# Kernel optimization log

Measured on AMD Instinct MI355X. Metric: run time of the kernel, lower is better.

Reference implementation:

```python
import jax, jax.numpy as jnp
import numpy as np

N_NODES = 100000
N_REL = 5
IN_F = 128
HID = 128

def _glorot(key, shape):
    fan_in, fan_out = shape[-2], shape[-1]
    s = jnp.sqrt(6.0 / (fan_in + fan_out))
    return jax.random.uniform(key, shape, jnp.float32, -s, s)

def setup_inputs() -> dict:
    key = jax.random.key(0)
    ks = jax.random.split(key, 16)
    x = jax.random.normal(ks[0], (N_NODES, IN_F), jnp.float32)
    edge_index = jax.random.randint(ks[1], (2, 1600000), 0, N_NODES, jnp.int32)
    edge_type = jax.random.randint(ks[2], (1600000,), 0, N_REL, jnp.int32)
    d = {"x": x, "edge_index": edge_index, "edge_type": edge_type}
    dims = [(IN_F, HID), (HID, HID), (HID, HID)]
    for li, (fi, fo) in enumerate(dims, start=1):
        d[f"W{li}"] = _glorot(ks[3 * li], (N_REL, fi, fo))        # per-relation weights
        d[f"root{li}"] = _glorot(ks[3 * li + 1], (fi, fo))        # root/self weight
        d[f"b{li}"] = jnp.zeros((fo,), jnp.float32)               # bias
    return d

def _rgcn_conv(x, src, dst, edge_type, W, root, b):
    # out = x @ root + b + sum_r segment_mean_r(x[src] @ W_r -> dst)
    out = x @ root + b
    for r in range(N_REL):  # small fixed relation count
        m = (edge_type == r).astype(x.dtype)                      # [E]
        h = (x @ W[r])[src] * m[:, None]                          # [E, out]
        s = jax.ops.segment_sum(h, dst, num_segments=N_NODES)     # [N, out]
        c = jax.ops.segment_sum(m, dst, num_segments=N_NODES)     # [N]
        out = out + s / jnp.maximum(c, 1.0)[:, None]
    return out

def reference(x, edge_index, edge_type, W1, root1, b1, W2, root2, b2, W3, root3, b3):
    src, dst = edge_index[0], edge_index[1]
    # dropout is identity in eval mode; applied as identity here
    h = jax.nn.relu(_rgcn_conv(x, src, dst, edge_type, W1, root1, b1))
    h = jax.nn.relu(_rgcn_conv(h, src, dst, edge_type, W2, root2, b2))
    h = jax.nn.relu(_rgcn_conv(h, src, dst, edge_type, W3, root3, b3))
    return h
```

## Files before the change

### kernel.cpp

```cpp
#include <hip/hip_runtime.h>

#define N_NODES_C 100000
#define N_REL_C 5
#define N_TOT (N_REL_C * N_NODES_C)
#define FEAT 128
#define KTOT 768
#define BM 128
#define GBK 64
#define NPART 2048

typedef __attribute__((ext_vector_type(8))) short bf16x8;
typedef __attribute__((ext_vector_type(4))) float f32x4;

__device__ inline unsigned short f2bf(float f) {
    union { float f; unsigned int u; } v; v.f = f;
    return (unsigned short)((v.u + 0x7FFFu + ((v.u >> 16) & 1u)) >> 16);
}

__device__ __forceinline__ unsigned int cvt_pk_bf16(float lo, float hi) {
    unsigned int r;
    asm("v_cvt_pk_bf16_f32 %0, %1, %2" : "=v"(r) : "v"(lo), "v"(hi));
    return r;
}

__device__ __forceinline__ void g2l16(const void* g, void* l) {
    __builtin_amdgcn_global_load_lds((const __attribute__((address_space(1))) unsigned int*)g,
                                     (__attribute__((address_space(3))) unsigned int*)l,
                                     16, 0, 0);
}

__device__ __forceinline__ void acc8(float (&a)[8], uint4 u) {
    union { unsigned int u; float f; } t;
    t.u = u.x << 16;         a[0] += t.f;
    t.u = u.x & 0xFFFF0000u; a[1] += t.f;
    t.u = u.y << 16;         a[2] += t.f;
    t.u = u.y & 0xFFFF0000u; a[3] += t.f;
    t.u = u.z << 16;         a[4] += t.f;
    t.u = u.z & 0xFFFF0000u; a[5] += t.f;
    t.u = u.w << 16;         a[6] += t.f;
    t.u = u.w & 0xFFFF0000u; a[7] += t.f;
}

__global__ __launch_bounds__(256) void count_part(const int* __restrict__ dst,
                                                  const int* __restrict__ et,
                                                  int* __restrict__ cnt, int E) {
    int cls = blockIdx.x & 7;
    int base = (blockIdx.x >> 3) * 256 + threadIdx.x;
    int stride = (gridDim.x >> 3) << 8;
    for (int e = base; e < E; e += stride) {
        int key = et[e] * N_NODES_C + dst[e];
        if ((key >> 16) == cls) atomicAdd(&cnt[key], 1);
    }
}

__global__ __launch_bounds__(256) void fill_part(const int* __restrict__ src,
                                                 const int* __restrict__ dst,
                                                 const int* __restrict__ et,
                                                 int* __restrict__ cursor,
                                                 int* __restrict__ esrc, int E) {
    int cls = blockIdx.x & 7;
    int base = (blockIdx.x >> 3) * 256 + threadIdx.x;
    int stride = (gridDim.x >> 3) << 8;
    for (int e = base; e < E; e += stride) {
        int key = et[e] * N_NODES_C + dst[e];
        if ((key >> 16) == cls) {
            int pos = atomicAdd(&cursor[key], 1);
            esrc[pos] = src[e];
        }
    }
}

__global__ __launch_bounds__(256) void make_inv(const int* __restrict__ cnt,
                                                float* __restrict__ inv, int n) {
    int i = blockIdx.x * 256 + threadIdx.x;
    if (i < n) inv[i] = 1.0f / (float)(cnt[i] > 1 ? cnt[i] : 1);
}

__global__ __launch_bounds__(256) void scan_block(const int* __restrict__ cnt,
                                                  int* __restrict__ rowptr,
                                                  int* __restrict__ bsum, int n) {
    __shared__ int sh[256];
    int tid = threadIdx.x;
    int i = blockIdx.x * 256 + tid;
    int v = (i < n) ? cnt[i] : 0;
    sh[tid] = v;
    __syncthreads();
#pragma unroll
    for (int o = 1; o < 256; o <<= 1) {
        int t = (tid >= o) ? sh[tid - o] : 0;
        __syncthreads();
        sh[tid] += t;
        __syncthreads();
    }
    if (i < n) rowptr[i] = sh[tid] - v;
    if (tid == 255) bsum[blockIdx.x] = sh[255];
}

__global__ __launch_bounds__(256) void scan_bsum(int* __restrict__ bsum, int nb) {
    __shared__ int sh[256];
    __shared__ int carry;
    int tid = threadIdx.x;
    if (tid == 0) carry = 0;
    __syncthreads();
    for (int base = 0; base < nb; base += 256) {
        int i = base + tid;
        int v = (i < nb) ? bsum[i] : 0;
        sh[tid] = v;
        __syncthreads();
#pragma unroll
        for (int o = 1; o < 256; o <<= 1) {
            int t = (tid >= o) ? sh[tid - o] : 0;
            __syncthreads();
            sh[tid] += t;
            __syncthreads();
        }
        int excl = sh[tid] - v + carry;
        int chunk_total = sh[255];
        __syncthreads();
        if (i < nb) bsum[i] = excl;
        if (tid == 0) carry += chunk_total;
        __syncthreads();
    }
}

__global__ __launch_bounds__(256) void scan_add(int* __restrict__ rowptr,
                                                const int* __restrict__ bsum,
                                                int n, int Etot) {
    int i = blockIdx.x * 256 + threadIdx.x;
    if (i < n) rowptr[i] += bsum[blockIdx.x];
    if (i == 0) rowptr[n] = Etot;
}

__global__ __launch_bounds__(256) void convert_x(const float* __restrict__ x,
                                                 unsigned short* __restrict__ xb, int n4) {
    int i = blockIdx.x * 256 + threadIdx.x;
    if (i >= n4) return;
    float4 v = ((const float4*)x)[i];
    ushort4 o;
    o.x = f2bf(v.x); o.y = f2bf(v.y); o.z = f2bf(v.z); o.w = f2bf(v.w);
    ((ushort4*)xb)[i] = o;
}

__global__ __launch_bounds__(256) void convert_w(const float* __restrict__ root,
                                                 const float* __restrict__ W,
                                                 unsigned short* __restrict__ Bt) {
    int idx = blockIdx.x * 256 + threadIdx.x;
    if (idx >= FEAT * KTOT) return;
    int c = idx / KTOT;
    int kv = idx - c * KTOT;
    float val;
    if (kv < FEAT) {
        val = root[kv * FEAT + c];
    } else {
        int r = (kv - FEAT) >> 7;
        int kk = (kv - FEAT) & 127;
        val = W[((size_t)r * FEAT + kk) * FEAT + c];
    }
    Bt[idx] = f2bf(val);
}

__global__ __launch_bounds__(256) void gather_mean(const unsigned short* __restrict__ hb,
                                                   const int* __restrict__ esrc,
                                                   const int* __restrict__ rowptr,
                                                   const float* __restrict__ inv,
                                                   unsigned short* __restrict__ agg,
                                                   int chunk0, int CL) {
    int qw = threadIdx.x >> 4;
    int seg = threadIdx.x & 15;
    int local = blockIdx.x * 16 + qw;
    if (local >= CL) return;
    int r = blockIdx.y;
    int node = chunk0 + local;
    int lo = rowptr[r * N_NODES_C + node];
    int hi = rowptr[r * N_NODES_C + node + 1];

    float a0[8], a1[8];
#pragma unroll
    for (int j = 0; j < 8; j++) { a0[j] = 0.f; a1[j] = 0.f; }

    const unsigned short* hseg = hb + seg * 8;

    int e = lo;
    for (; e + 4 <= hi; e += 4) {
        int s0 = esrc[e];
        int s1 = esrc[e + 1];
        int s2 = esrc[e + 2];
        int s3 = esrc[e + 3];
        uint4 u0 = *(const uint4*)(hseg + ((size_t)s0 << 7));
        uint4 u1 = *(const uint4*)(hseg + ((size_t)s1 << 7));
        uint4 u2 = *(const uint4*)(hseg + ((size_t)s2 << 7));
        uint4 u3 = *(const uint4*)(hseg + ((size_t)s3 << 7));
        acc8(a0, u0);
        acc8(a1, u1);
        acc8(a0, u2);
        acc8(a1, u3);
    }
    if (e + 2 <= hi) {
        int s0 = esrc[e];
        int s1 = esrc[e + 1];
        uint4 u0 = *(const uint4*)(hseg + ((size_t)s0 << 7));
        uint4 u1 = *(const uint4*)(hseg + ((size_t)s1 << 7));
        acc8(a0, u0);
        acc8(a1, u1);
        e += 2;
    }
    if (e < hi) {
        int s = esrc[e];
        uint4 u = *(const uint4*)(hseg + ((size_t)s << 7));
        acc8(a0, u);
    }

    float sc = inv[r * N_NODES_C + node];
    uint4 o;
    o.x = cvt_pk_bf16((a0[0] + a1[0]) * sc, (a0[1] + a1[1]) * sc);
    o.y = cvt_pk_bf16((a0[2] + a1[2]) * sc, (a0[3] + a1[3]) * sc);
    o.z = cvt_pk_bf16((a0[4] + a1[4]) * sc, (a0[5] + a1[5]) * sc);
    o.w = cvt_pk_bf16((a0[6] + a1[6]) * sc, (a0[7] + a1[7]) * sc);
    *(uint4*)(agg + (((size_t)r * CL + local) << 7) + seg * 8) = o;
}

__global__ __launch_bounds__(256) void rgcn_gemm(const unsigned short* __restrict__ hb,
                                                 const unsigned short* __restrict__ agg,
                                                 const unsigned short* __restrict__ Bt,
                                                 const float* __restrict__ bias,
                                                 float* __restrict__ outf,
                                                 unsigned short* __restrict__ outb,
                                                 int chunk0, int CL) {
    __shared__ unsigned short As[BM * GBK];
    __shared__ unsigned short Bs[FEAT * GBK];

    const int tid = threadIdx.x;
    const int w = tid >> 6, lane = tid & 63;
    const int wr = w >> 1, wc = w & 1;
    const int lm = lane & 15, lq = lane >> 4;
    const int brow0 = blockIdx.x * BM;

    f32x4 acc[4][4];
#pragma unroll
    for (int i = 0; i < 4; i++)
#pragma unroll
        for (int j = 0; j < 4; j++) acc[i][j] = (f32x4){0.f, 0.f, 0.f, 0.f};

    size_t hboff[4];
    size_t aggoff[4];
    size_t boff[4];
    int ldsbase[4];
#pragma unroll
    for (int i = 0; i < 4; i++) {
        int cid = (w * 4 + i) * 64 + lane;
        int row = cid >> 3;
        int cs = (cid & 7) ^ (row & 7);
        int gr = brow0 + row;
        if (gr >= CL) gr = CL - 1;
        hboff[i]  = ((size_t)(chunk0 + gr) << 7) + cs * 8;
        aggoff[i] = ((size_t)gr << 7) + cs * 8;
        boff[i]   = (size_t)row * KTOT + cs * 8;
        ldsbase[i] = ((w * 4 + i) * 64) * 8;
    }

    for (int kb = 0; kb < KTOT; kb += GBK) {
        __syncthreads();
        if (kb < FEAT) {
#pragma unroll
            for (int i = 0; i < 4; i++)
                g2l16(hb + hboff[i] + kb, &As[ldsbase[i]]);
        } else {
            size_t reloff = (((size_t)((kb - FEAT) >> 7)) * CL << 7) + (size_t)((kb - FEAT) & 127);
#pragma unroll
            for (int i = 0; i < 4; i++)
                g2l16(agg + aggoff[i] + reloff, &As[ldsbase[i]]);
        }
#pragma unroll
        for (int i = 0; i < 4; i++)
            g2l16(Bt + boff[i] + kb, &Bs[ldsbase[i]]);
        __syncthreads();

#pragma unroll
        for (int h = 0; h < 2; h++) {
            bf16x8 af[4], bf[4];
#pragma unroll
            for (int t = 0; t < 4; t++) {
                int row = wr * 64 + t * 16 + lm;
                int ca = (h * 4 + lq) ^ (row & 7);
                af[t] = *(const bf16x8*)&As[row * GBK + ca * 8];
                int col = wc * 64 + t * 16 + lm;
                int cb = (h * 4 + lq) ^ (col & 7);
                bf[t] = *(const bf16x8*)&Bs[col * GBK + cb * 8];
            }
#pragma unroll
            for (int i = 0; i < 4; i++)
#pragma unroll
                for (int j = 0; j < 4; j++)
                    acc[i][j] = __builtin_amdgcn_mfma_f32_16x16x32_bf16(af[i], bf[j], acc[i][j], 0, 0, 0);
        }
    }

    float bcol[4];
#pragma unroll
    for (int j = 0; j < 4; j++) bcol[j] = bias[wc * 64 + j * 16 + lm];

#pragma unroll
    for (int i = 0; i < 4; i++) {
#pragma unroll
        for (int reg = 0; reg < 4; reg++) {
            int lr = brow0 + wr * 64 + i * 16 + lq * 4 + reg;
            if (lr < CL) {
                size_t grow = (size_t)(chunk0 + lr) << 7;
#pragma unroll
                for (int j = 0; j < 4; j++) {
                    float v = acc[i][j][reg] + bcol[j];
                    v = fmaxf(v, 0.f);
                    int col = wc * 64 + j * 16 + lm;
                    if (outf) outf[grow + col] = v;
                    else outb[grow + col] = f2bf(v);
                }
            }
        }
    }
}

extern "C" void kernel_launch(void* const* d_in, const int* in_sizes, int n_in,
                              void* d_out, int out_size, void* d_ws, size_t ws_size,
                              hipStream_t stream) {
    const float* x = (const float*)d_in[0];
    const int* ei  = (const int*)d_in[1];
    const int* et  = (const int*)d_in[2];
    const int E = in_sizes[2];
    const int* src  = ei;
    const int* dstp = ei + E;

    int CL = 25000;
    if (ws_size >= 61997056ull + 100000ull * 1280ull + 589824ull) CL = 100000;
    else if (ws_size >= 61997056ull + 50000ull * 1280ull + 589824ull) CL = 50000;
    const int NCHUNK = N_NODES_C / CL;

    char* ws = (char*)d_ws;
    float* inv             = (float*)ws;
    int*   rowptr          = (int*)(ws + 2097152);
    int*   esrc            = (int*)(ws + 4194304);
    unsigned short* xbA    = (unsigned short*)(ws + 10616832);
    unsigned short* xbB    = (unsigned short*)(ws + 36306944);
    unsigned short* agg    = (unsigned short*)(ws + 61997056);
    unsigned short* BtAll  = (unsigned short*)(ws + 61997056 + (size_t)CL * 1280ull);
    int*   cnt    = (int*)(ws + 61997056);
    int*   cursor = (int*)(ws + 61997056 + 2097152);
    int*   bsum   = (int*)(ws + 61997056 + 4194304);

    const int nscan_blocks = (N_TOT + 255) / 256;

    hipMemsetAsync(cnt, 0, (size_t)N_TOT * 4, stream);
    count_part<<<NPART, 256, 0, stream>>>(dstp, et, cnt, E);
    make_inv<<<(N_TOT + 255) / 256, 256, 0, stream>>>(cnt, inv, N_TOT);
    scan_block<<<nscan_blocks, 256, 0, stream>>>(cnt, rowptr, bsum, N_TOT);
    scan_bsum<<<1, 256, 0, stream>>>(bsum, nscan_blocks);
    scan_add<<<nscan_blocks, 256, 0, stream>>>(rowptr, bsum, N_TOT, E);
    hipMemcpyAsync(cursor, rowptr, (size_t)N_TOT * 4, hipMemcpyDeviceToDevice, stream);
    fill_part<<<NPART, 256, 0, stream>>>(src, dstp, et, cursor, esrc, E);

    const int n4 = N_NODES_C * FEAT / 4;
    convert_x<<<(n4 + 255) / 256, 256, 0, stream>>>(x, xbA, n4);

    const float* Wp[3] = {(const float*)d_in[3], (const float*)d_in[6], (const float*)d_in[9]};
    const float* Rp[3] = {(const float*)d_in[4], (const float*)d_in[7], (const float*)d_in[10]};
    const float* Bp[3] = {(const float*)d_in[5], (const float*)d_in[8], (const float*)d_in[11]};

    const int nw = FEAT * KTOT;
    for (int l = 0; l < 3; l++)
        convert_w<<<(nw + 255) / 256, 256, 0, stream>>>(Rp[l], Wp[l],
                                                        BtAll + (size_t)l * nw);

    const int gemm_grid = (CL + BM - 1) / BM;
    dim3 ggrid((CL + 15) / 16, N_REL_C);

    for (int l = 0; l < 3; l++) {
        const unsigned short* hin = (l == 1) ? xbB : xbA;
        unsigned short* outb = (l == 0) ? xbB : ((l == 1) ? xbA : nullptr);
        float* outf = (l == 2) ? (float*)d_out : nullptr;
        for (int c = 0; c < NCHUNK; c++) {
            gather_mean<<<ggrid, 256, 0, stream>>>(hin, esrc, rowptr, inv, agg,
                                                   c * CL, CL);
            rgcn_gemm<<<gemm_grid, 256, 0, stream>>>(hin, agg, BtAll + (size_t)l * nw,
                                                     Bp[l], outf, outb, c * CL, CL);
        }
    }
}
```

Before: 651.1 us.

## Precompute edge keys, fuse preprocessing kernels, and pack gather accumulation as float2

A new kernel computes the edge key (relation*N + dst) once, so count and fill passes read one array instead of recomputing it from two. make_inv is folded into scan_block, the rowptr-to-cursor device copy is folded into scan_add, and the three weight-conversion launches become a single 2D launch. Gather accumulation now uses float2 pairs, which may allow packed fp32 adds. This trims launches and redundant memory passes in the preprocessing stage, at the cost of an extra key buffer in the workspace and a higher workspace threshold for choosing large chunks.

```diff
diff --git a/kernel.cpp b/kernel.cpp
--- a/kernel.cpp
+++ b/kernel.cpp
@@ -29,60 +29,66 @@
                                      16, 0, 0);
 }
 
-__device__ __forceinline__ void acc8(float (&a)[8], uint4 u) {
+__device__ __forceinline__ void accp(float2 (&a)[4], uint4 u) {
     union { unsigned int u; float f; } t;
-    t.u = u.x << 16;         a[0] += t.f;
-    t.u = u.x & 0xFFFF0000u; a[1] += t.f;
-    t.u = u.y << 16;         a[2] += t.f;
-    t.u = u.y & 0xFFFF0000u; a[3] += t.f;
-    t.u = u.z << 16;         a[4] += t.f;
-    t.u = u.z & 0xFFFF0000u; a[5] += t.f;
-    t.u = u.w << 16;         a[6] += t.f;
-    t.u = u.w & 0xFFFF0000u; a[7] += t.f;
-}
-
-__global__ __launch_bounds__(256) void count_part(const int* __restrict__ dst,
-                                                  const int* __restrict__ et,
+    float2 v;
+    t.u = u.x << 16;         v.x = t.f;
+    t.u = u.x & 0xFFFF0000u; v.y = t.f;
+    a[0] += v;
+    t.u = u.y << 16;         v.x = t.f;
+    t.u = u.y & 0xFFFF0000u; v.y = t.f;
+    a[1] += v;
+    t.u = u.z << 16;         v.x = t.f;
+    t.u = u.z & 0xFFFF0000u; v.y = t.f;
+    a[2] += v;
+    t.u = u.w << 16;         v.x = t.f;
+    t.u = u.w & 0xFFFF0000u; v.y = t.f;
+    a[3] += v;
+}
+
+__global__ __launch_bounds__(256) void prep_key(const int* __restrict__ dst,
+                                                const int* __restrict__ et,
+                                                int* __restrict__ key, int E) {
+    int e = blockIdx.x * 256 + threadIdx.x;
+    if (e < E) key[e] = et[e] * N_NODES_C + dst[e];
+}
+
+__global__ __launch_bounds__(256) void count_part(const int* __restrict__ key,
                                                   int* __restrict__ cnt, int E) {
     int cls = blockIdx.x & 7;
     int base = (blockIdx.x >> 3) * 256 + threadIdx.x;
     int stride = (gridDim.x >> 3) << 8;
     for (int e = base; e < E; e += stride) {
-        int key = et[e] * N_NODES_C + dst[e];
-        if ((key >> 16) == cls) atomicAdd(&cnt[key], 1);
+        int k = key[e];
+        if ((k >> 16) == cls) atomicAdd(&cnt[k], 1);
     }
 }
 
 __global__ __launch_bounds__(256) void fill_part(const int* __restrict__ src,
-                                                 const int* __restrict__ dst,
-                                                 const int* __restrict__ et,
+                                                 const int* __restrict__ key,
                                                  int* __restrict__ cursor,
                                                  int* __restrict__ esrc, int E) {
     int cls = blockIdx.x & 7;
     int base = (blockIdx.x >> 3) * 256 + threadIdx.x;
     int stride = (gridDim.x >> 3) << 8;
     for (int e = base; e < E; e += stride) {
-        int key = et[e] * N_NODES_C + dst[e];
-        if ((key >> 16) == cls) {
-            int pos = atomicAdd(&cursor[key], 1);
+        int k = key[e];
+        if ((k >> 16) == cls) {
+            int pos = atomicAdd(&cursor[k], 1);
             esrc[pos] = src[e];
         }
     }
-}
-
-__global__ __launch_bounds__(256) void make_inv(const int* __restrict__ cnt,
-                                                float* __restrict__ inv, int n) {
-    int i = blockIdx.x * 256 + threadIdx.x;
-    if (i < n) inv[i] = 1.0f / (float)(cnt[i] > 1 ? cnt[i] : 1);
 }
 
 __global__ __launch_bounds__(256) void scan_block(const int* __restrict__ cnt,
                                                   int* __restrict__ rowptr,
-                                                  int* __restrict__ bsum, int n) {
+                                                  int* __restrict__ bsum,
+                                                  float* __restrict__ inv, int n) {
     __shared__ int sh[256];
     int tid = threadIdx.x;
     int i = blockIdx.x * 256 + tid;
     int v = (i < n) ? cnt[i] : 0;
+    if (i < n) inv[i] = 1.0f / (float)(v > 1 ? v : 1);
     sh[tid] = v;
     __syncthreads();
 #pragma unroll
@@ -124,10 +130,15 @@
 }
 
 __global__ __launch_bounds__(256) void scan_add(int* __restrict__ rowptr,
+                                                int* __restrict__ cursor,
                                                 const int* __restrict__ bsum,
                                                 int n, int Etot) {
     int i = blockIdx.x * 256 + threadIdx.x;
-    if (i < n) rowptr[i] += bsum[blockIdx.x];
+    if (i < n) {
+        int v = rowptr[i] + bsum[blockIdx.x];
+        rowptr[i] = v;
+        cursor[i] = v;
+    }
     if (i == 0) rowptr[n] = Etot;
 }
 
@@ -141,11 +152,18 @@
     ((ushort4*)xb)[i] = o;
 }
 
-__global__ __launch_bounds__(256) void convert_w(const float* __restrict__ root,
-                                                 const float* __restrict__ W,
-                                                 unsigned short* __restrict__ Bt) {
+__global__ __launch_bounds__(256) void convert_w3(const float* __restrict__ r0,
+                                                  const float* __restrict__ w0,
+                                                  const float* __restrict__ r1,
+                                                  const float* __restrict__ w1,
+                                                  const float* __restrict__ r2,
+                                                  const float* __restrict__ w2,
+                                                  unsigned short* __restrict__ BtAll) {
     int idx = blockIdx.x * 256 + threadIdx.x;
     if (idx >= FEAT * KTOT) return;
+    int l = blockIdx.y;
+    const float* root = (l == 0) ? r0 : ((l == 1) ? r1 : r2);
+    const float* W    = (l == 0) ? w0 : ((l == 1) ? w1 : w2);
     int c = idx / KTOT;
     int kv = idx - c * KTOT;
     float val;
@@ -156,7 +174,7 @@
         int kk = (kv - FEAT) & 127;
         val = W[((size_t)r * FEAT + kk) * FEAT + c];
     }
-    Bt[idx] = f2bf(val);
+    BtAll[(size_t)l * FEAT * KTOT + idx] = f2bf(val);
 }
 
 __global__ __launch_bounds__(256) void gather_mean(const unsigned short* __restrict__ hb,
@@ -174,9 +192,12 @@
     int lo = rowptr[r * N_NODES_C + node];
     int hi = rowptr[r * N_NODES_C + node + 1];
 
-    float a0[8], a1[8];
-#pragma unroll
-    for (int j = 0; j < 8; j++) { a0[j] = 0.f; a1[j] = 0.f; }
+    float2 a0[4], a1[4];
+#pragma unroll
+    for (int j = 0; j < 4; j++) {
+        a0[j] = make_float2(0.f, 0.f);
+        a1[j] = make_float2(0.f, 0.f);
+    }
 
     const unsigned short* hseg = hb + seg * 8;
 
@@ -190,32 +211,37 @@
         uint4 u1 = *(const uint4*)(hseg + ((size_t)s1 << 7));
         uint4 u2 = *(const uint4*)(hseg + ((size_t)s2 << 7));
         uint4 u3 = *(const uint4*)(hseg + ((size_t)s3 << 7));
-        acc8(a0, u0);
-        acc8(a1, u1);
-        acc8(a0, u2);
-        acc8(a1, u3);
+        accp(a0, u0);
+        accp(a1, u1);
+        accp(a0, u2);
+        accp(a1, u3);
     }
     if (e + 2 <= hi) {
         int s0 = esrc[e];
         int s1 = esrc[e + 1];
         uint4 u0 = *(const uint4*)(hseg + ((size_t)s0 << 7));
         uint4 u1 = *(const uint4*)(hseg + ((size_t)s1 << 7));
-        acc8(a0, u0);
-        acc8(a1, u1);
+        accp(a0, u0);
+        accp(a1, u1);
         e += 2;
     }
     if (e < hi) {
         int s = esrc[e];
         uint4 u = *(const uint4*)(hseg + ((size_t)s << 7));
-        acc8(a0, u);
+        accp(a0, u);
     }
 
     float sc = inv[r * N_NODES_C + node];
+    float2 s;
     uint4 o;
-    o.x = cvt_pk_bf16((a0[0] + a1[0]) * sc, (a0[1] + a1[1]) * sc);
-    o.y = cvt_pk_bf16((a0[2] + a1[2]) * sc, (a0[3] + a1[3]) * sc);
-    o.z = cvt_pk_bf16((a0[4] + a1[4]) * sc, (a0[5] + a1[5]) * sc);
-    o.w = cvt_pk_bf16((a0[6] + a1[6]) * sc, (a0[7] + a1[7]) * sc);
+    s.x = a0[0].x + a1[0].x; s.y = a0[0].y + a1[0].y;
+    o.x = cvt_pk_bf16(s.x * sc, s.y * sc);
+    s.x = a0[1].x + a1[1].x; s.y = a0[1].y + a1[1].y;
+    o.y = cvt_pk_bf16(s.x * sc, s.y * sc);
+    s.x = a0[2].x + a1[2].x; s.y = a0[2].y + a1[2].y;
+    o.z = cvt_pk_bf16(s.x * sc, s.y * sc);
+    s.x = a0[3].x + a1[3].x; s.y = a0[3].y + a1[3].y;
+    o.w = cvt_pk_bf16(s.x * sc, s.y * sc);
     *(uint4*)(agg + (((size_t)r * CL + local) << 7) + seg * 8) = o;
 }
 
@@ -330,8 +356,8 @@
     const int* dstp = ei + E;
 
     int CL = 25000;
-    if (ws_size >= 61997056ull + 100000ull * 1280ull + 589824ull) CL = 100000;
-    else if (ws_size >= 61997056ull + 50000ull * 1280ull + 589824ull) CL = 50000;
+    if (ws_size >= 61997056ull + 100000ull * 1280ull + 1769472ull) CL = 100000;
+    else if (ws_size >= 61997056ull + 50000ull * 1280ull + 1769472ull) CL = 50000;
     const int NCHUNK = N_NODES_C / CL;
 
     char* ws = (char*)d_ws;
@@ -345,29 +371,28 @@
     int*   cnt    = (int*)(ws + 61997056);
     int*   cursor = (int*)(ws + 61997056 + 2097152);
     int*   bsum   = (int*)(ws + 61997056 + 4194304);
+    int*   key    = (int*)(ws + 61997056 + 8388608);
 
     const int nscan_blocks = (N_TOT + 255) / 256;
 
     hipMemsetAsync(cnt, 0, (size_t)N_TOT * 4, stream);
-    count_part<<<NPART, 256, 0, stream>>>(dstp, et, cnt, E);
-    make_inv<<<(N_TOT + 255) / 256, 256, 0, stream>>>(cnt, inv, N_TOT);
-    scan_block<<<nscan_blocks, 256, 0, stream>>>(cnt, rowptr, bsum, N_TOT);
+    prep_key<<<(E + 255) / 256, 256, 0, stream>>>(dstp, et, key, E);
+    count_part<<<NPART, 256, 0, stream>>>(key, cnt, E);
+    scan_block<<<nscan_blocks, 256, 0, stream>>>(cnt, rowptr, bsum, inv, N_TOT);
     scan_bsum<<<1, 256, 0, stream>>>(bsum, nscan_blocks);
-    scan_add<<<nscan_blocks, 256, 0, stream>>>(rowptr, bsum, N_TOT, E);
-    hipMemcpyAsync(cursor, rowptr, (size_t)N_TOT * 4, hipMemcpyDeviceToDevice, stream);
-    fill_part<<<NPART, 256, 0, stream>>>(src, dstp, et, cursor, esrc, E);
+    scan_add<<<nscan_blocks, 256, 0, stream>>>(rowptr, cursor, bsum, N_TOT, E);
+    fill_part<<<NPART, 256, 0, stream>>>(src, key, cursor, esrc, E);
 
     const int n4 = N_NODES_C * FEAT / 4;
     convert_x<<<(n4 + 255) / 256, 256, 0, stream>>>(x, xbA, n4);
 
-    const float* Wp[3] = {(const float*)d_in[3], (const float*)d_in[6], (const float*)d_in[9]};
-    const float* Rp[3] = {(const float*)d_in[4], (const float*)d_in[7], (const float*)d_in[10]};
+    const int nw = FEAT * KTOT;
+    convert_w3<<<dim3((nw + 255) / 256, 3), 256, 0, stream>>>(
+        (const float*)d_in[4], (const float*)d_in[3],
+        (const float*)d_in[7], (const float*)d_in[6],
+        (const float*)d_in[10], (const float*)d_in[9], BtAll);
+
     const float* Bp[3] = {(const float*)d_in[5], (const float*)d_in[8], (const float*)d_in[11]};
-
-    const int nw = FEAT * KTOT;
-    for (int l = 0; l < 3; l++)
-        convert_w<<<(nw + 255) / 256, 256, 0, stream>>>(Rp[l], Wp[l],
-                                                        BtAll + (size_t)l * nw);
 
     const int gemm_grid = (CL + BM - 1) / BM;
     dim3 ggrid((CL + 15) / 16, N_REL_C);
```

Result: no change. 644.7 us (-1.0%).
